# Kernel tuning notes

Measured on AMD Instinct MI355X. Metric: run time of the kernel, lower is better.

Reference implementation:

```python
import jax, jax.numpy as jnp
import numpy as np

B, T, C = 2, 2048, 1024
NH, HS = 16, 64  # n_heads, head_size; NH*HS == C


def setup_inputs() -> dict:
    key = jax.random.key(0)
    k1, k2, k3 = jax.random.split(key, 3)
    x = jax.random.normal(k1, (B, T, C), dtype=jnp.float32)
    W_attn = jax.random.normal(k2, (C, 3 * C), dtype=jnp.float32) * (C ** -0.5)
    b_attn = jax.random.normal(k3, (3 * C,), dtype=jnp.float32) * 0.02
    return {"x": x, "W_attn": W_attn, "b_attn": b_attn}


def reference(x, W_attn, b_attn):
    Bv, Tv, Cv = x.shape
    qkv = x @ W_attn + b_attn                       # [B,T,3C]
    q, k, v = jnp.split(qkv, 3, axis=-1)            # each [B,T,C]
    q = q.reshape(Bv, Tv, NH, HS)
    k = k.reshape(Bv, Tv, NH, HS)
    v = v.reshape(Bv, Tv, NH, HS)
    scale = HS ** -0.5
    wei = jnp.einsum('bqhd,bkhd->bhqk', q, k) * scale  # [B,H,T,T]
    causal = jnp.tril(jnp.ones((Tv, Tv), dtype=bool))
    wei = jnp.where(causal[None, None], wei, -jnp.inf)
    wei = jax.nn.softmax(wei, axis=-1)
    # dropout layers are identity in eval mode
    out = jnp.einsum('bhqk,bkhd->bqhd', wei, v)     # [B,T,H,HS]
    return out.reshape(Bv, Tv, Cv)
```

## Files before the change

kernel.cpp:

```cpp
#include <hip/hip_runtime.h>
#include <hip/hip_bf16.h>
#include <math.h>

#define BB   2
#define TT   2048
#define CC   1024
#define NH   16
#define HS   64
#define N3C  3072
#define MM   4096

typedef __attribute__((ext_vector_type(8))) short bf16x8;
typedef __attribute__((ext_vector_type(4))) float f32x4;

#define NINF (-__builtin_inff())
#define QSCALE 0.125f

__device__ __forceinline__ unsigned short f2bf(float f) {
    unsigned int u = __builtin_bit_cast(unsigned int, f);
    unsigned int r = u + 0x7fffu + ((u >> 16) & 1u);
    return (unsigned short)(r >> 16);
}

__device__ __forceinline__ unsigned short f2bf_fast(float f) {
    unsigned int u = __builtin_bit_cast(unsigned int, f);
    return (unsigned short)((u + 0x8000u) >> 16);
}

__device__ __forceinline__ void gl_lds16(const unsigned short* g, unsigned short* l) {
    __builtin_amdgcn_global_load_lds(
        (const __attribute__((address_space(1))) unsigned int*)g,
        (__attribute__((address_space(3))) unsigned int*)l, 16, 0, 0);
}

__global__ __launch_bounds__(256) void k_cast(const float* __restrict__ x,
                                              unsigned short* __restrict__ xb) {
    int i = (blockIdx.x * 256 + threadIdx.x) * 4;
    float4 v = *(const float4*)(x + i);
    ushort4 o;
    o.x = f2bf(v.x); o.y = f2bf(v.y); o.z = f2bf(v.z); o.w = f2bf(v.w);
    *(ushort4*)(xb + i) = o;
}

__global__ __launch_bounds__(256) void k_transpose_w(const float* __restrict__ W,
                                                     unsigned short* __restrict__ Wt) {
    __shared__ float tile[32][33];
    const int n0 = blockIdx.x * 32;
    const int k0 = blockIdx.y * 32;
    const int t = threadIdx.x;
    {
        int kr = t >> 3, ns = (t & 7) * 4;
        float4 v = *(const float4*)(W + (size_t)(k0 + kr) * N3C + n0 + ns);
        tile[kr][ns + 0] = v.x; tile[kr][ns + 1] = v.y;
        tile[kr][ns + 2] = v.z; tile[kr][ns + 3] = v.w;
    }
    __syncthreads();
    {
        int nr = t >> 3, ks = (t & 7) * 4;
        ushort4 o;
        o.x = f2bf(tile[ks + 0][nr]);
        o.y = f2bf(tile[ks + 1][nr]);
        o.z = f2bf(tile[ks + 2][nr]);
        o.w = f2bf(tile[ks + 3][nr]);
        *(ushort4*)(Wt + (size_t)(n0 + nr) * CC + k0 + ks) = o;
    }
}

#define EPS 72

__global__ __launch_bounds__(256) void k_gemm_qkv(const unsigned short* __restrict__ xb,
                                                  const unsigned short* __restrict__ wt,
                                                  const float* __restrict__ bias,
                                                  unsigned short* __restrict__ qb,
                                                  unsigned short* __restrict__ kb,
                                                  unsigned short* __restrict__ vt) {
    __shared__ unsigned short sA[128 * 32];
    __shared__ unsigned short sB[128 * 32];
    __shared__ unsigned short sE[4 * 64 * EPS];
    const int t = threadIdx.x;
    const int wave = t >> 6, lane = t & 63;
    const int quad = lane >> 4, c16 = lane & 15;
    const int wm = wave >> 1, wn = wave & 1;
    const int m0 = blockIdx.y * 128;
    const int n0 = blockIdx.x * 128;
    const int sel = n0 >> 10;

    f32x4 acc[4][4];
#pragma unroll
    for (int i = 0; i < 4; ++i)
#pragma unroll
        for (int j = 0; j < 4; ++j) acc[i][j] = f32x4{0, 0, 0, 0};

    const int srow = wave * 16 + (lane >> 2);
    const int scol = (lane & 3) * 8;
    const unsigned short* gA = xb + (size_t)(m0 + srow) * CC + scol;
    const unsigned short* gB = wt + (size_t)(n0 + srow) * CC + scol;
    unsigned short* lA = sA + wave * 512 + lane * 8;
    unsigned short* lB = sB + wave * 512 + lane * 8;

    for (int k0 = 0; k0 < CC; k0 += 32) {
        __syncthreads();
        gl_lds16(gA + k0, lA);
        gl_lds16(gA + k0 + (size_t)64 * CC, lA + 2048);
        gl_lds16(gB + k0, lB);
        gl_lds16(gB + k0 + (size_t)64 * CC, lB + 2048);
        __syncthreads();
        bf16x8 a[4], b[4];
#pragma unroll
        for (int rt = 0; rt < 4; ++rt)
            a[rt] = *(const bf16x8*)(sA + (wm * 64 + rt * 16 + c16) * 32 + quad * 8);
#pragma unroll
        for (int ct = 0; ct < 4; ++ct)
            b[ct] = *(const bf16x8*)(sB + (wn * 64 + ct * 16 + c16) * 32 + quad * 8);
#pragma unroll
        for (int rt = 0; rt < 4; ++rt)
#pragma unroll
            for (int ct = 0; ct < 4; ++ct)
                acc[rt][ct] = __builtin_amdgcn_mfma_f32_16x16x32_bf16(b[ct], a[rt], acc[rt][ct], 0, 0, 0);
    }

    const int head = ((n0 + wn * 64) >> 6) & 15;
    const int bh = (m0 >> 11) * NH + head;
    const int tbase = (m0 & 2047) + wm * 64;
    if (sel < 2) {
        unsigned short* dst = (sel == 0) ? qb : kb;
        const float sc = (sel == 0) ? QSCALE : 1.0f;
        unsigned short* ew = sE + wave * (64 * EPS);
#pragma unroll
        for (int ct = 0; ct < 4; ++ct) {
            const float4 bv4 = *(const float4*)(bias + n0 + wn * 64 + ct * 16 + quad * 4);
            const int d0 = ct * 16 + quad * 4;
#pragma unroll
            for (int rt = 0; rt < 4; ++rt) {
                ushort4 pk;
                pk.x = f2bf((acc[rt][ct][0] + bv4.x) * sc);
                pk.y = f2bf((acc[rt][ct][1] + bv4.y) * sc);
                pk.z = f2bf((acc[rt][ct][2] + bv4.z) * sc);
                pk.w = f2bf((acc[rt][ct][3] + bv4.w) * sc);
                *(ushort4*)(ew + (rt * 16 + c16) * EPS + d0) = pk;
            }
        }
        const size_t gbase = ((size_t)bh * TT + tbase) * HS;
#pragma unroll
        for (int i = 0; i < 8; ++i) {
            const int trow = i * 8 + (lane >> 3);
            bf16x8 row = *(const bf16x8*)(ew + trow * EPS + (lane & 7) * 8);
            *(bf16x8*)(dst + gbase + (size_t)trow * HS + (lane & 7) * 8) = row;
        }
    } else {
#pragma unroll
        for (int ct = 0; ct < 4; ++ct) {
            const float4 bv4 = *(const float4*)(bias + n0 + wn * 64 + ct * 16 + quad * 4);
#pragma unroll
            for (int r = 0; r < 4; ++r) {
                const int d = ct * 16 + quad * 4 + r;
                const float bv = ((const float*)&bv4)[r];
#pragma unroll
                for (int rt = 0; rt < 4; ++rt) {
                    const int tt = tbase + rt * 16 + c16;
                    vt[((size_t)bh * HS + d) * TT + tt] = f2bf(acc[rt][ct][r] + bv);
                }
            }
        }
    }
}

#define SPP 72

__global__ __launch_bounds__(512) void k_attn(const unsigned short* __restrict__ qb,
                                              const unsigned short* __restrict__ kb,
                                              const unsigned short* __restrict__ vt,
                                              float* __restrict__ out) {
    __shared__ unsigned short sK[2][64 * 64];
    __shared__ unsigned short sV[2][64 * 64];
    __shared__ unsigned short sP[8][16 * SPP];

    const int tid = threadIdx.x;
    const int wave = tid >> 6, lane = tid & 63;
    const int quad = lane >> 4, c16 = lane & 15;
    const int g = blockIdx.x >> 5;
    const int bh = blockIdx.x & 31;

    const unsigned short* Qp = qb + (size_t)bh * TT * HS;
    const unsigned short* Kp = kb + (size_t)bh * TT * HS;
    const unsigned short* Vp = vt + (size_t)bh * HS * TT;

    unsigned short* sPw = sP[wave];

    const int srow = tid >> 3;
    const int ssc = tid & 7;
    const int sl = (ssc ^ (srow & 7)) * 8;
    const unsigned short* Ksrc = Kp + (size_t)srow * HS + sl;
    const unsigned short* Vsrc = Vp + (size_t)srow * TT + sl;
    auto stage = [&](int buf, int kt) {
        const int kb0 = kt * 64;
        gl_lds16(Ksrc + (size_t)kb0 * HS, &sK[buf][tid * 8]);
        gl_lds16(Vsrc + kb0, &sV[buf][tid * 8]);
    };

    const int b_ = bh >> 4, h_ = bh & 15;

#pragma unroll 1
    for (int ph = 0; ph < 2; ++ph) {
        const int p = ph ? g : (15 - g);
        const int qw = p * 128 + wave * 16;
        const int qmax = qw + 15;
        const int kiters = 2 * p + 2;

        bf16x8 qf[2];
#pragma unroll
        for (int ks = 0; ks < 2; ++ks)
            qf[ks] = *(const bf16x8*)(Qp + (size_t)(qw + c16) * HS + ks * 32 + quad * 8);

        f32x4 o[4];
#pragma unroll
        for (int dt = 0; dt < 4; ++dt) o[dt] = f32x4{0, 0, 0, 0};
        float lsum = 0.f;

        auto tile = [&](int buf, int kt) {
            const int kb0 = kt * 64;
            const unsigned short* Kb = sK[buf];
            const unsigned short* Vb = sV[buf];
            bf16x8 kf[4][2];
#pragma unroll
            for (int mt = 0; mt < 4; ++mt)
#pragma unroll
                for (int ks = 0; ks < 2; ++ks)
                    kf[mt][ks] = *(const bf16x8*)(Kb + (mt * 16 + c16) * 64 +
                                                  (((ks * 4 + quad) ^ (c16 & 7)) * 8));
            f32x4 s[4];
#pragma unroll
            for (int mt = 0; mt < 4; ++mt) s[mt] = f32x4{0, 0, 0, 0};
#pragma unroll
            for (int mt = 0; mt < 4; ++mt) {
                s[mt] = __builtin_amdgcn_mfma_f32_16x16x32_bf16(kf[mt][0], qf[0], s[mt], 0, 0, 0);
                s[mt] = __builtin_amdgcn_mfma_f32_16x16x32_bf16(kf[mt][1], qf[1], s[mt], 0, 0, 0);
            }
            bf16x8 vf[4][2];
#pragma unroll
            for (int dt = 0; dt < 4; ++dt)
#pragma unroll
                for (int ks = 0; ks < 2; ++ks)
                    vf[dt][ks] = *(const bf16x8*)(Vb + (dt * 16 + c16) * 64 +
                                                  (((ks * 4 + quad) ^ (c16 & 7)) * 8));
            const bool maskit = (kb0 + 63 > qw);
            const int rowq = qw + c16;
            float l = 0.f;
#pragma unroll
            for (int mt = 0; mt < 4; ++mt) {
                float p0, p1, p2, p3;
                if (maskit) {
                    const int k = kb0 + mt * 16 + quad * 4;
                    p0 = __expf((k     <= rowq) ? s[mt][0] : NINF);
                    p1 = __expf((k + 1 <= rowq) ? s[mt][1] : NINF);
                    p2 = __expf((k + 2 <= rowq) ? s[mt][2] : NINF);
                    p3 = __expf((k + 3 <= rowq) ? s[mt][3] : NINF);
                } else {
                    p0 = __expf(s[mt][0]);
                    p1 = __expf(s[mt][1]);
                    p2 = __expf(s[mt][2]);
                    p3 = __expf(s[mt][3]);
                }
                l += (p0 + p1) + (p2 + p3);
                ushort4 pk;
                pk.x = f2bf_fast(p0); pk.y = f2bf_fast(p1);
                pk.z = f2bf_fast(p2); pk.w = f2bf_fast(p3);
                *(ushort4*)(sPw + c16 * SPP + mt * 16 + quad * 4) = pk;
            }
            lsum += l;
            bf16x8 pf[2];
#pragma unroll
            for (int ks = 0; ks < 2; ++ks)
                pf[ks] = *(const bf16x8*)(sPw + c16 * SPP + ks * 32 + quad * 8);
#pragma unroll
            for (int dt = 0; dt < 4; ++dt) {
                o[dt] = __builtin_amdgcn_mfma_f32_16x16x32_bf16(vf[dt][0], pf[0], o[dt], 0, 0, 0);
                o[dt] = __builtin_amdgcn_mfma_f32_16x16x32_bf16(vf[dt][1], pf[1], o[dt], 0, 0, 0);
            }
        };

        stage(0, 0);
        for (int kt = 0; kt < kiters; ++kt) {
            if (kt + 1 < kiters) {
                stage((kt + 1) & 1, kt + 1);
                asm volatile("s_waitcnt vmcnt(2)" ::: "memory");
            } else {
                asm volatile("s_waitcnt vmcnt(0)" ::: "memory");
            }
            __builtin_amdgcn_s_barrier();
            asm volatile("" ::: "memory");
            if (kt * 64 <= qmax) tile(kt & 1, kt);
            __builtin_amdgcn_s_barrier();
            asm volatile("" ::: "memory");
        }

        lsum += __shfl_xor(lsum, 16);
        lsum += __shfl_xor(lsum, 32);

        const float il = 1.0f / lsum;
        const int q = qw + c16;
        float* orow = out + ((size_t)(b_ * TT + q)) * CC + h_ * HS;
#pragma unroll
        for (int dt = 0; dt < 4; ++dt) {
            float4 w;
            w.x = o[dt][0] * il; w.y = o[dt][1] * il;
            w.z = o[dt][2] * il; w.w = o[dt][3] * il;
            *(float4*)(orow + dt * 16 + quad * 4) = w;
        }
    }
}

extern "C" void kernel_launch(void* const* d_in, const int* in_sizes, int n_in,
                              void* d_out, int out_size, void* d_ws, size_t ws_size,
                              hipStream_t stream) {
    const float* x    = (const float*)d_in[0];
    const float* W    = (const float*)d_in[1];
    const float* bias = (const float*)d_in[2];
    float* out = (float*)d_out;

    char* ws = (char*)d_ws;
    unsigned short* xb = (unsigned short*)(ws);
    unsigned short* wt = (unsigned short*)(ws + 8388608);
    unsigned short* qb = (unsigned short*)(ws + 8388608 + 6291456);
    unsigned short* kb = (unsigned short*)(ws + 8388608 + 6291456 + 8388608);
    unsigned short* vt = (unsigned short*)(ws + 8388608 + 6291456 + 2 * 8388608);

    k_cast<<<dim3(MM * CC / (256 * 4)), dim3(256), 0, stream>>>(x, xb);
    k_transpose_w<<<dim3(N3C / 32, CC / 32), dim3(256), 0, stream>>>(W, wt);
    k_gemm_qkv<<<dim3(N3C / 128, MM / 128), dim3(256), 0, stream>>>(xb, wt, bias, qb, kb, vt);
    k_attn<<<dim3(8 * 32), dim3(512), 0, stream>>>(qb, kb, vt, out);
}
```

Baseline: 168.3 us.

## Widen QKV GEMM K-tile to 64 with XOR-swizzled LDS and staged V-transpose stores

The QKV projection GEMM now loads 64-wide K slices per iteration, halving the loop trip count and barrier count. The LDS layout is XOR-swizzled to avoid bank conflicts on the MFMA fragment reads. The A/B staging buffers and the epilogue buffer are aliased into one shared array, so the extra K width does not raise LDS use. The V-transpose epilogue, which did scattered 2-byte global stores, now stages through LDS and writes 16-byte coalesced rows. The aliasing needs an extra barrier before the epilogue.

```diff
diff --git a/kernel.cpp b/kernel.cpp
--- a/kernel.cpp
+++ b/kernel.cpp
@@ -74,9 +74,11 @@
                                                   unsigned short* __restrict__ qb,
                                                   unsigned short* __restrict__ kb,
                                                   unsigned short* __restrict__ vt) {
-    __shared__ unsigned short sA[128 * 32];
-    __shared__ unsigned short sB[128 * 32];
-    __shared__ unsigned short sE[4 * 64 * EPS];
+    __shared__ unsigned short smem[4 * 64 * EPS];
+    unsigned short* sA = smem;
+    unsigned short* sB = smem + 128 * 64;
+    unsigned short* sE = smem;
+
     const int t = threadIdx.x;
     const int wave = t >> 6, lane = t & 63;
     const int quad = lane >> 4, c16 = lane & 15;
@@ -91,33 +93,38 @@
 #pragma unroll
         for (int j = 0; j < 4; ++j) acc[i][j] = f32x4{0, 0, 0, 0};
 
-    const int srow = wave * 16 + (lane >> 2);
-    const int scol = (lane & 3) * 8;
-    const unsigned short* gA = xb + (size_t)(m0 + srow) * CC + scol;
-    const unsigned short* gB = wt + (size_t)(n0 + srow) * CC + scol;
-    unsigned short* lA = sA + wave * 512 + lane * 8;
-    unsigned short* lB = sB + wave * 512 + lane * 8;
-
-    for (int k0 = 0; k0 < CC; k0 += 32) {
+    const int srow_ = t >> 3;
+    const int sslot = t & 7;
+
+    for (int k0 = 0; k0 < CC; k0 += 64) {
         __syncthreads();
-        gl_lds16(gA + k0, lA);
-        gl_lds16(gA + k0 + (size_t)64 * CC, lA + 2048);
-        gl_lds16(gB + k0, lB);
-        gl_lds16(gB + k0 + (size_t)64 * CC, lB + 2048);
+#pragma unroll
+        for (int rnd = 0; rnd < 4; ++rnd) {
+            const int row = rnd * 32 + srow_;
+            const int sl = (sslot ^ (row & 7)) * 8;
+            gl_lds16(xb + (size_t)(m0 + row) * CC + k0 + sl, sA + rnd * 2048 + t * 8);
+            gl_lds16(wt + (size_t)(n0 + row) * CC + k0 + sl, sB + rnd * 2048 + t * 8);
+        }
         __syncthreads();
-        bf16x8 a[4], b[4];
-#pragma unroll
-        for (int rt = 0; rt < 4; ++rt)
-            a[rt] = *(const bf16x8*)(sA + (wm * 64 + rt * 16 + c16) * 32 + quad * 8);
-#pragma unroll
-        for (int ct = 0; ct < 4; ++ct)
-            b[ct] = *(const bf16x8*)(sB + (wn * 64 + ct * 16 + c16) * 32 + quad * 8);
-#pragma unroll
-        for (int rt = 0; rt < 4; ++rt)
+#pragma unroll
+        for (int ks = 0; ks < 2; ++ks) {
+            bf16x8 a[4], b[4];
+#pragma unroll
+            for (int rt = 0; rt < 4; ++rt)
+                a[rt] = *(const bf16x8*)(sA + (wm * 64 + rt * 16 + c16) * 64 +
+                                         (((ks * 4 + quad) ^ (c16 & 7)) * 8));
 #pragma unroll
             for (int ct = 0; ct < 4; ++ct)
-                acc[rt][ct] = __builtin_amdgcn_mfma_f32_16x16x32_bf16(b[ct], a[rt], acc[rt][ct], 0, 0, 0);
-    }
+                b[ct] = *(const bf16x8*)(sB + (wn * 64 + ct * 16 + c16) * 64 +
+                                         (((ks * 4 + quad) ^ (c16 & 7)) * 8));
+#pragma unroll
+            for (int rt = 0; rt < 4; ++rt)
+#pragma unroll
+                for (int ct = 0; ct < 4; ++ct)
+                    acc[rt][ct] = __builtin_amdgcn_mfma_f32_16x16x32_bf16(b[ct], a[rt], acc[rt][ct], 0, 0, 0);
+        }
+    }
+    __syncthreads();
 
     const int head = ((n0 + wn * 64) >> 6) & 15;
     const int bh = (m0 >> 11) * NH + head;
@@ -148,6 +155,7 @@
             *(bf16x8*)(dst + gbase + (size_t)trow * HS + (lane & 7) * 8) = row;
         }
     } else {
+        unsigned short* ew = sE + wave * (64 * EPS);
 #pragma unroll
         for (int ct = 0; ct < 4; ++ct) {
             const float4 bv4 = *(const float4*)(bias + n0 + wn * 64 + ct * 16 + quad * 4);
@@ -156,11 +164,16 @@
                 const int d = ct * 16 + quad * 4 + r;
                 const float bv = ((const float*)&bv4)[r];
 #pragma unroll
-                for (int rt = 0; rt < 4; ++rt) {
-                    const int tt = tbase + rt * 16 + c16;
-                    vt[((size_t)bh * HS + d) * TT + tt] = f2bf(acc[rt][ct][r] + bv);
-                }
-            }
+                for (int rt = 0; rt < 4; ++rt)
+                    ew[d * EPS + rt * 16 + c16] = f2bf(acc[rt][ct][r] + bv);
+            }
+        }
+        const size_t vbase = (size_t)bh * HS * TT + tbase;
+#pragma unroll
+        for (int i = 0; i < 8; ++i) {
+            const int d = i * 8 + (lane >> 3);
+            bf16x8 row = *(const bf16x8*)(ew + d * EPS + (lane & 7) * 8);
+            *(bf16x8*)(vt + vbase + (size_t)d * TT + (lane & 7) * 8) = row;
         }
     }
 }
```

Measured after the change: 162.0 us. 3.7% less time.
